# Performance work log

Measured on AMD Instinct MI355X. Metric: run time of the kernel, lower is better.

## Reference

```python
import jax, jax.numpy as jnp
import numpy as np
from jax import lax

B, T, V, D, H = 32, 128, 32000, 512, 512


def setup_inputs() -> dict:
    key = jax.random.key(0)
    ks = jax.random.split(key, 8)
    s = 0.05  # keep gate pre-activations in a sane range
    return {
        "dst": jax.random.randint(ks[0], (B, T), 0, V),
        "E": jax.random.normal(ks[1], (V, D), jnp.float32) * s,
        "W_ih": jax.random.normal(ks[2], (4 * H, D + H), jnp.float32) * s,
        "W_hh": jax.random.normal(ks[3], (4 * H, H), jnp.float32) * s,
        "b_ih": jnp.zeros((4 * H,), jnp.float32),
        "b_hh": jnp.zeros((4 * H,), jnp.float32),
        "h0": jax.random.normal(ks[4], (B, H), jnp.float32) * s,
        "c0": jax.random.normal(ks[5], (B, H), jnp.float32) * s,
        "out0": jax.random.normal(ks[6], (B, H), jnp.float32) * s,
    }


def reference(dst, E, W_ih, W_hh, b_ih, b_hh, h0, c0, out0):
    # Embed targets: [B, T, D] -> time-major [T, B, D]
    emb_tbd = jnp.swapaxes(E[dst], 0, 1)

    def step(carry, e_t):
        h, c, out_prev = carry
        # input feeding: concat embedding with previous output -> [B, D+H]
        x = jnp.concatenate([e_t, out_prev], axis=1)
        gates = x @ W_ih.T + b_ih + h @ W_hh.T + b_hh  # [B, 4H]
        i, f, g, o = jnp.split(gates, 4, axis=1)
        i = jax.nn.sigmoid(i)
        f = jax.nn.sigmoid(f)
        g = jnp.tanh(g)
        o = jax.nn.sigmoid(o)
        c_new = f * c + i * g
        h_new = o * jnp.tanh(c_new)
        # attn is identity; dropout disabled (p=0 / eval)
        return (h_new, c_new, h_new), h_new

    _, outs_tbh = lax.scan(step, (h0, c0, out0), emb_tbd)  # [T, B, H]
    out_bth = jnp.swapaxes(outs_tbh, 0, 1)  # [B, T, H]
    # weight-tied projection to vocab + log softmax
    logits = jnp.einsum("bth,vh->btv", out_bth, E)  # [B, T, V]
    return jax.nn.log_softmax(logits, axis=-1)
```

## Files before the change

### kernel.cpp

```cpp
#include <hip/hip_runtime.h>
#include <hip/hip_bf16.h>
#include <math.h>

#define B_ 32
#define T_ 128
#define V_ 32000
#define D_ 512
#define H_ 512

typedef __attribute__((ext_vector_type(8))) short bf16x8;
typedef __attribute__((ext_vector_type(4))) float f32x4;
typedef __attribute__((ext_vector_type(2))) unsigned long long u64x2;

#define AS1 __attribute__((address_space(1)))
#define AS3 __attribute__((address_space(3)))

__device__ __forceinline__ unsigned short f2bf(float x) {
  unsigned int b = __float_as_uint(x);
  return (unsigned short)((b + 0x7FFFu + ((b >> 16) & 1u)) >> 16);
}
__device__ __forceinline__ float bf2f(unsigned short u) {
  return __uint_as_float(((unsigned int)u) << 16);
}
__device__ __forceinline__ float sigm(float x) { return 1.0f / (1.0f + __expf(-x)); }
__device__ __forceinline__ float tanh_fast(float x) { return 1.0f - 2.0f / (__expf(2.0f * x) + 1.0f); }

__device__ __forceinline__ unsigned long long ald64(const unsigned long long* p) {
  return __hip_atomic_load(p, __ATOMIC_RELAXED, __HIP_MEMORY_SCOPE_AGENT);
}
__device__ __forceinline__ unsigned ald32(const unsigned* p) {
  return __hip_atomic_load(p, __ATOMIC_RELAXED, __HIP_MEMORY_SCOPE_AGENT);
}

__global__ __launch_bounds__(64) void embed_bf_kernel(const int* __restrict__ dst,
                                                      const float* __restrict__ E,
                                                      unsigned short* __restrict__ embbf) {
  int rt = blockIdx.x;
  int t = rt >> 5, b = rt & 31;
  int v = dst[b * T_ + t];
  const float4* src = (const float4*)(E + (size_t)v * D_);
  ushort4* d = (ushort4*)(embbf + (size_t)rt * D_);
  #pragma unroll
  for (int r = 0; r < 2; ++r) {
    float4 x = src[threadIdx.x + r * 64];
    ushort4 o; o.x = f2bf(x.x); o.y = f2bf(x.y); o.z = f2bf(x.z); o.w = f2bf(x.w);
    d[threadIdx.x + r * 64] = o;
  }
}

__global__ void cvt_kernel(const float* __restrict__ in, unsigned short* __restrict__ out, int n4) {
  int stride = gridDim.x * blockDim.x;
  for (int i = blockIdx.x * blockDim.x + threadIdx.x; i < n4; i += stride) {
    float4 v = ((const float4*)in)[i];
    ushort4 o; o.x = f2bf(v.x); o.y = f2bf(v.y); o.z = f2bf(v.z); o.w = f2bf(v.w);
    ((ushort4*)out)[i] = o;
  }
}

__global__ void cvt_w1_kernel(const float* __restrict__ Wih, unsigned short* __restrict__ W1bf, int n4) {
  int stride = gridDim.x * blockDim.x;
  for (int i = blockIdx.x * blockDim.x + threadIdx.x; i < n4; i += stride) {
    int flat = i * 4;
    int r = flat >> 9, c = flat & 511;
    float4 v = *(const float4*)(Wih + (size_t)r * 1024 + c);
    ushort4 o; o.x = f2bf(v.x); o.y = f2bf(v.y); o.z = f2bf(v.z); o.w = f2bf(v.w);
    ((ushort4*)W1bf)[i] = o;
  }
}

__global__ void wr_prep_swz_kernel(const float* __restrict__ Wih, const float* __restrict__ Whh,
                                   unsigned short* __restrict__ Wrs, int n4) {
  int stride = gridDim.x * blockDim.x;
  for (int i = blockIdx.x * blockDim.x + threadIdx.x; i < n4; i += stride) {
    int flat = i * 4;
    int grow = flat >> 9, k = flat & 511;
    float4 a = *(const float4*)(Wih + (size_t)grow * 1024 + 512 + k);
    float4 b = ((const float4*)Whh)[i];
    ushort4 o;
    o.x = f2bf(a.x + b.x); o.y = f2bf(a.y + b.y); o.z = f2bf(a.z + b.z); o.w = f2bf(a.w + b.w);
    int gate = grow >> 9, kgl = grow & 511;
    int orow = (kgl >> 5) * 128 + (kgl & 31) * 4 + gate;
    int chunk = (k >> 3) ^ (orow & 7);
    *(ushort4*)(Wrs + (size_t)orow * 512 + chunk * 8 + (k & 7)) = o;
  }
}

__global__ __launch_bounds__(256) void gemm_pre_kernel(
    const unsigned short* __restrict__ A,
    const unsigned short* __restrict__ Bm,
    const float* __restrict__ bih, const float* __restrict__ bhh,
    unsigned short* __restrict__ preA3)
{
  __shared__ unsigned short ldsA[2][128 * 32];
  __shared__ unsigned short ldsB[2][128 * 32];
  const int tid = threadIdx.x;
  const int lane = tid & 63;
  const int wid = tid >> 6;
  const int wm = wid >> 1, wn = wid & 1;
  const int m0 = blockIdx.y * 128;
  const int n0 = blockIdx.x * 128;
  const int srow = lane >> 2;
  const int scol = (lane & 3) * 8;

  f32x4 acc[4][4] = {};
  const int NK = 512 / 32;

  auto stage = [&](int kk, int buf) {
    const int k0 = kk * 32;
    #pragma unroll
    for (int c = 0; c < 2; ++c) {
      const int r = wid * 32 + c * 16;
      const unsigned short* sa = A  + (size_t)(m0 + r + srow) * 512 + k0 + scol;
      const unsigned short* sb = Bm + (size_t)(n0 + r + srow) * 512 + k0 + scol;
      __builtin_amdgcn_global_load_lds((const AS1 void*)sa, (AS3 void*)&ldsA[buf][r * 32], 16, 0, 0);
      __builtin_amdgcn_global_load_lds((const AS1 void*)sb, (AS3 void*)&ldsB[buf][r * 32], 16, 0, 0);
    }
  };

  stage(0, 0);
  __syncthreads();

  const int rl = lane & 15;
  const int kb = lane >> 4;

  for (int kk = 0; kk < NK; ++kk) {
    const int buf = kk & 1;
    if (kk + 1 < NK) stage(kk + 1, buf ^ 1);
    const bf16x8* Af = (const bf16x8*)&ldsA[buf][0];
    const bf16x8* Bf = (const bf16x8*)&ldsB[buf][0];
    bf16x8 av[4], bv[4];
    #pragma unroll
    for (int mi = 0; mi < 4; ++mi) av[mi] = Af[(wm * 64 + mi * 16 + rl) * 4 + kb];
    #pragma unroll
    for (int ni = 0; ni < 4; ++ni) bv[ni] = Bf[(wn * 64 + ni * 16 + rl) * 4 + kb];
    #pragma unroll
    for (int mi = 0; mi < 4; ++mi)
      #pragma unroll
      for (int ni = 0; ni < 4; ++ni)
        acc[mi][ni] = __builtin_amdgcn_mfma_f32_16x16x32_bf16(av[mi], bv[ni], acc[mi][ni], 0, 0, 0);
    __syncthreads();
  }

  const int rb = (lane >> 4) * 4;
  #pragma unroll
  for (int mi = 0; mi < 4; ++mi)
    #pragma unroll
    for (int ni = 0; ni < 4; ++ni) {
      int mbase = m0 + wm * 64 + mi * 16 + rb;
      int col   = n0 + wn * 64 + ni * 16 + rl;
      int gate = col >> 9, kg = col & 511;
      int tt = mbase >> 5, bb0 = mbase & 31;
      float bb = bih[col] + bhh[col];
      #pragma unroll
      for (int j = 0; j < 4; ++j)
        preA3[(((size_t)tt * 512 + kg) * 32 + bb0 + j) * 4 + gate] = f2bf(acc[mi][ni][j] + bb);
    }
}

__global__ __launch_bounds__(256) void delta0_kernel(const float* __restrict__ Wih,
                                                     const float* __restrict__ out0,
                                                     const float* __restrict__ h0,
                                                     unsigned short* __restrict__ preA3) {
  const int r = blockIdx.x;
  const int tid = threadIdx.x;
  const int b = tid >> 3, seg = tid & 7;
  __shared__ float red[32][9];
  const float4* o4 = (const float4*)(out0 + (size_t)b * 512 + seg * 64);
  const float4* h4 = (const float4*)(h0 + (size_t)b * 512 + seg * 64);
  const float4* w4 = (const float4*)(Wih + (size_t)r * 1024 + 512 + seg * 64);
  float s = 0.f;
  #pragma unroll
  for (int j = 0; j < 16; ++j) {
    float4 o = o4[j], h = h4[j], w = w4[j];
    s += (o.x - h.x) * w.x + (o.y - h.y) * w.y + (o.z - h.z) * w.z + (o.w - h.w) * w.w;
  }
  red[b][seg] = s;
  __syncthreads();
  if (tid < 32) {
    float t = 0.f;
    #pragma unroll
    for (int j = 0; j < 8; ++j) t += red[tid][j];
    int gate = r >> 9, kgl = r & 511;
    unsigned short* p = preA3 + ((size_t)kgl * 32 + tid) * 4 + gate;
    *p = f2bf(bf2f(*p) + t);
  }
}

__global__ __launch_bounds__(1024) void lstm_persist_rs_kernel(
    const unsigned short* __restrict__ Wrs,
    const unsigned short* __restrict__ preA3,
    const float* __restrict__ c0,
    unsigned short* __restrict__ hb0,
    unsigned short* __restrict__ hb1,
    unsigned short* __restrict__ Abf,
    unsigned int* __restrict__ flags)
{
  __shared__ unsigned short wlds[128 * 512];
  __shared__ __align__(16) char hexch[2][16 * 1024];
  const int tid = threadIdx.x, bid = blockIdx.x;
  const int lane = tid & 63, wid = tid >> 6;

  #pragma unroll
  for (int it = 0; it < 8; ++it) {
    int r = it * 16 + wid;
    const unsigned short* src = Wrs + ((size_t)bid * 128 + r) * 512 + lane * 8;
    __builtin_amdgcn_global_load_lds((const AS1 void*)src, (AS3 void*)&wlds[r * 512], 16, 0, 0);
  }

  const int myhalf = wid >> 3;
  const int rt = wid & 7;
  const int q = lane >> 4, rl = lane & 15;
  const int kg = bid * 32 + rt * 4 + q;
  const int b = myhalf * 16 + rl;
  float c_reg = c0[(size_t)b * 512 + kg];

  const int row = rt * 16 + rl;
  const char* wbase = (const char*)wlds + row * 1024;
  const int rx = (row & 7) << 4;
  const int hx = (rl & 7) << 4;

  const int sw = wid & 7;
  const int sr = sw * 2 + (lane >> 5);
  const int sc = lane & 31;
  const int sblk = sc >> 1;
  const int srx = (sr & 7) << 4;
  const int sofs = sc * 32;

  if (myhalf == 0) {
    const unsigned long long* src =
        (const unsigned long long*)(hb0 + (size_t)sr * 512) + sc * 4;
    unsigned long long d0 = ald64(src + 0), d1 = ald64(src + 1);
    unsigned long long d2 = ald64(src + 2), d3 = ald64(src + 3);
    char* dst = hexch[0] + sr * 1024;
    u64x2 w0; w0[0] = d0; w0[1] = d1;
    u64x2 w1; w1[0] = d2; w1[1] = d3;
    *(u64x2*)(dst + (sofs ^ srx)) = w0;
    *(u64x2*)(dst + ((sofs + 16) ^ srx)) = w1;
  }
  __syncthreads();

  for (int p = 0; p < 2 * T_; ++p) {
    const int t = p >> 1, ph = p & 1, buf = p & 1;

    if (myhalf == ph) {
      unsigned long long pre =
          *(const unsigned long long*)(preA3 + (((size_t)t * 512 + kg) * 32 + b) * 4);
      const char* hbase = hexch[buf] + rl * 1024;
      f32x4 acc = {}, acc2 = {};
      #pragma unroll
      for (int kk = 0; kk < 16; kk += 2) {
        int k0 = kk * 32 + q * 8;
        int k1 = k0 + 32;
        bf16x8 av0 = *(const bf16x8*)(wbase + ((k0 * 2) ^ rx));
        bf16x8 bv0 = *(const bf16x8*)(hbase + ((k0 * 2) ^ hx));
        bf16x8 av1 = *(const bf16x8*)(wbase + ((k1 * 2) ^ rx));
        bf16x8 bv1 = *(const bf16x8*)(hbase + ((k1 * 2) ^ hx));
        acc  = __builtin_amdgcn_mfma_f32_16x16x32_bf16(av0, bv0, acc, 0, 0, 0);
        acc2 = __builtin_amdgcn_mfma_f32_16x16x32_bf16(av1, bv1, acc2, 0, 0, 0);
      }
      float g0 = acc[0] + acc2[0] + bf2f((unsigned short)(pre));
      float g1 = acc[1] + acc2[1] + bf2f((unsigned short)(pre >> 16));
      float g2 = acc[2] + acc2[2] + bf2f((unsigned short)(pre >> 32));
      float g3 = acc[3] + acc2[3] + bf2f((unsigned short)(pre >> 48));
      float iv = sigm(g0), fv = sigm(g1), gv = tanh_fast(g2), ov = sigm(g3);
      float cn = fv * c_reg + iv * gv;
      c_reg = cn;
      float hn = ov * tanh_fast(cn);
      int hv = (int)f2bf(hn);
      int nb = __shfl(hv, lane + 16);
      if ((q & 1) == 0) {
        unsigned pair = (unsigned)hv | ((unsigned)nb << 16);
        if (t != T_ - 1) {
          unsigned short* hout = ((t + 1) & 1) ? hb1 : hb0;
          __hip_atomic_store((unsigned int*)(hout + (size_t)b * 512 + kg), pair,
                             __ATOMIC_RELAXED, __HIP_MEMORY_SCOPE_AGENT);
        }
        *(unsigned*)(Abf + ((size_t)b * T_ + t) * 512 + kg) = pair;
      }
    } else if (p + 1 < 2 * T_) {
      const int t2 = (p + 1) >> 1;
      if (t2 > 0) {
        const unsigned* fl = &flags[(myhalf * 16 + sblk) * 16];
        unsigned spins = 0;
        while (ald32(fl) < (unsigned)t2) {
          if (++spins > 1000000u) break;
        }
      }
      const unsigned short* hsrc = (t2 & 1) ? hb1 : hb0;
      const unsigned long long* src =
          (const unsigned long long*)(hsrc + (size_t)(myhalf * 16 + sr) * 512) + sc * 4;
      unsigned long long d0 = ald64(src + 0), d1 = ald64(src + 1);
      unsigned long long d2 = ald64(src + 2), d3 = ald64(src + 3);
      char* dst = hexch[buf ^ 1] + sr * 1024;
      u64x2 w0; w0[0] = d0; w0[1] = d1;
      u64x2 w1; w1[0] = d2; w1[1] = d3;
      *(u64x2*)(dst + (sofs ^ srx)) = w0;
      *(u64x2*)(dst + ((sofs + 16) ^ srx)) = w1;
    }

    __syncthreads();

    if (tid == ph * 512)
      __hip_atomic_store(&flags[(ph * 16 + bid) * 16], (unsigned)(t + 1),
                         __ATOMIC_RELAXED, __HIP_MEMORY_SCOPE_AGENT);
  }
}

__global__ __launch_bounds__(256) void gemm_kernel(
    const unsigned short* __restrict__ A,
    const unsigned short* __restrict__ Bm,
    float* __restrict__ C,
    float* __restrict__ pmax, float* __restrict__ psum)
{
  __shared__ unsigned short ldsA[2][128 * 32];
  __shared__ unsigned short ldsB[2][128 * 32];
  __shared__ float smax[2][128];
  __shared__ float ssum[2][128];
  const int tid = threadIdx.x;
  const int lane = tid & 63;
  const int wid = tid >> 6;
  const int wm = wid >> 1, wn = wid & 1;
  const int m0 = blockIdx.x * 128;
  const int n0 = blockIdx.y * 128;
  const int srow = lane >> 2;

  f32x4 acc[4][4] = {};
  const int NK = 512 / 32;

  auto stage = [&](int kk, int buf) {
    const int k0 = kk * 32;
    const int sw = (srow >> 1) & 3;
    const int gc = ((lane & 3) ^ sw) * 8;
    #pragma unroll
    for (int c = 0; c < 2; ++c) {
      const int r = wid * 32 + c * 16;
      const unsigned short* sa = A  + (size_t)(m0 + r + srow) * 512 + k0 + gc;
      const unsigned short* sb = Bm + (size_t)(n0 + r + srow) * 512 + k0 + gc;
      __builtin_amdgcn_global_load_lds((const AS1 void*)sa, (AS3 void*)&ldsA[buf][r * 32], 16, 0, 0);
      __builtin_amdgcn_global_load_lds((const AS1 void*)sb, (AS3 void*)&ldsB[buf][r * 32], 16, 0, 0);
    }
  };

  stage(0, 0);
  __syncthreads();

  const int rl = lane & 15;
  const int kb = lane >> 4;
  const int rsw = kb ^ ((rl >> 1) & 3);

  for (int kk = 0; kk < NK; ++kk) {
    const int buf = kk & 1;
    if (kk + 1 < NK) stage(kk + 1, buf ^ 1);
    const bf16x8* Af = (const bf16x8*)&ldsA[buf][0];
    const bf16x8* Bf = (const bf16x8*)&ldsB[buf][0];
    bf16x8 av[4], bv[4];
    #pragma unroll
    for (int mi = 0; mi < 4; ++mi) av[mi] = Af[(wm * 64 + mi * 16 + rl) * 4 + rsw];
    #pragma unroll
    for (int ni = 0; ni < 4; ++ni) bv[ni] = Bf[(wn * 64 + ni * 16 + rl) * 4 + rsw];
    #pragma unroll
    for (int mi = 0; mi < 4; ++mi)
      #pragma unroll
      for (int ni = 0; ni < 4; ++ni)
        acc[mi][ni] = __builtin_amdgcn_mfma_f32_16x16x32_bf16(av[mi], bv[ni], acc[mi][ni], 0, 0, 0);
    __syncthreads();
  }

  const int rb = kb * 4;
  #pragma unroll
  for (int mi = 0; mi < 4; ++mi)
    #pragma unroll
    for (int ni = 0; ni < 4; ++ni) {
      size_t rrow = (size_t)(m0 + wm * 64 + mi * 16 + rb);
      size_t col = (size_t)(n0 + wn * 64 + ni * 16 + rl);
      #pragma unroll
      for (int j = 0; j < 4; ++j)
        __builtin_nontemporal_store(acc[mi][ni][j], &C[(rrow + j) * (size_t)V_ + col]);
    }

  float tm[4][4];
  #pragma unroll
  for (int mi = 0; mi < 4; ++mi)
    #pragma unroll
    for (int j = 0; j < 4; ++j) {
      float m = fmaxf(fmaxf(acc[mi][0][j], acc[mi][1][j]), fmaxf(acc[mi][2][j], acc[mi][3][j]));
      m = fmaxf(m, __shfl_xor(m, 1)); m = fmaxf(m, __shfl_xor(m, 2));
      m = fmaxf(m, __shfl_xor(m, 4)); m = fmaxf(m, __shfl_xor(m, 8));
      tm[mi][j] = m;
    }
  if (rl == 0) {
    #pragma unroll
    for (int mi = 0; mi < 4; ++mi)
      #pragma unroll
      for (int j = 0; j < 4; ++j)
        smax[wn][wm * 64 + mi * 16 + kb * 4 + j] = tm[mi][j];
  }
  __syncthreads();
  float ts[4][4];
  #pragma unroll
  for (int mi = 0; mi < 4; ++mi)
    #pragma unroll
    for (int j = 0; j < 4; ++j) {
      int rlocal = wm * 64 + mi * 16 + kb * 4 + j;
      float M = fmaxf(smax[0][rlocal], smax[1][rlocal]);
      float s = __expf(acc[mi][0][j] - M) + __expf(acc[mi][1][j] - M) +
                __expf(acc[mi][2][j] - M) + __expf(acc[mi][3][j] - M);
      s += __shfl_xor(s, 1); s += __shfl_xor(s, 2);
      s += __shfl_xor(s, 4); s += __shfl_xor(s, 8);
      ts[mi][j] = s;
    }
  if (rl == 0) {
    #pragma unroll
    for (int mi = 0; mi < 4; ++mi)
      #pragma unroll
      for (int j = 0; j < 4; ++j)
        ssum[wn][wm * 64 + mi * 16 + kb * 4 + j] = ts[mi][j];
  }
  __syncthreads();
  if (tid < 128) {
    float M = fmaxf(smax[0][tid], smax[1][tid]);
    float S = ssum[0][tid] + ssum[1][tid];
    pmax[(size_t)(m0 + tid) * 256 + blockIdx.y] = M;
    psum[(size_t)(m0 + tid) * 256 + blockIdx.y] = S;
  }
}

__global__ __launch_bounds__(256) void softmax_finish_kernel(
    float* __restrict__ C, const float* __restrict__ pmax, const float* __restrict__ psum) {
  const size_t row = blockIdx.x;
  const int tid = threadIdx.x, lane = tid & 63, wid = tid >> 6;
  __shared__ float red[4];

  float pm = (tid < 250) ? pmax[row * 256 + tid] : -INFINITY;
  float ps = (tid < 250) ? psum[row * 256 + tid] : 0.f;

  float m = pm;
  #pragma unroll
  for (int off = 32; off > 0; off >>= 1) m = fmaxf(m, __shfl_xor(m, off));
  if (lane == 0) red[wid] = m;
  __syncthreads();
  m = fmaxf(fmaxf(red[0], red[1]), fmaxf(red[2], red[3]));
  __syncthreads();

  float s = (tid < 250) ? ps * __expf(pm - m) : 0.f;
  #pragma unroll
  for (int off = 32; off > 0; off >>= 1) s += __shfl_xor(s, off);
  if (lane == 0) red[wid] = s;
  __syncthreads();
  s = red[0] + red[1] + red[2] + red[3];
  const float lse = m + logf(s);

  f32x4* p4 = (f32x4*)(C + row * (size_t)V_);
  for (int i = tid; i < 8000; i += 256) {
    f32x4 v = p4[i];
    v -= lse;
    __builtin_nontemporal_store(v, &p4[i]);
  }
}

extern "C" void kernel_launch(void* const* d_in, const int* in_sizes, int n_in,
                              void* d_out, int out_size, void* d_ws, size_t ws_size,
                              hipStream_t stream) {
  const int*   dst  = (const int*)d_in[0];
  const float* E    = (const float*)d_in[1];
  const float* Wih  = (const float*)d_in[2];
  const float* Whh  = (const float*)d_in[3];
  const float* bih  = (const float*)d_in[4];
  const float* bhh  = (const float*)d_in[5];
  const float* h0   = (const float*)d_in[6];
  const float* c0   = (const float*)d_in[7];
  const float* out0 = (const float*)d_in[8];
  float* C = (float*)d_out;

  char* ws = (char*)d_ws;
  unsigned short* Ebf   = (unsigned short*)(ws);
  unsigned short* preA3 = (unsigned short*)(ws + (size_t)33554432);
  unsigned short* Wrs   = (unsigned short*)(ws + (size_t)50331648);
  unsigned short* embbf = (unsigned short*)(ws + (size_t)52428800);
  float*          pmax  = (float*)(ws + (size_t)52428800);
  unsigned short* W1bf  = (unsigned short*)(ws + (size_t)56623104);
  float*          psum  = (float*)(ws + (size_t)56623104);
  unsigned short* Abf   = (unsigned short*)(ws + (size_t)60817408);
  unsigned short* hb0   = (unsigned short*)(ws + (size_t)65011712);
  unsigned short* hb1   = (unsigned short*)(ws + (size_t)65044480);
  unsigned int*   flg   = (unsigned int*)(ws + (size_t)65077248);

  (void)hipMemsetAsync(flg, 0, 2048, stream);

  embed_bf_kernel<<<dim3(T_ * B_), dim3(64), 0, stream>>>(dst, E, embbf);
  cvt_kernel<<<dim3(2048), dim3(256), 0, stream>>>(E, Ebf, V_ * D_ / 4);
  cvt_w1_kernel<<<dim3(256), dim3(256), 0, stream>>>(Wih, W1bf, 2048 * 512 / 4);
  wr_prep_swz_kernel<<<dim3(256), dim3(256), 0, stream>>>(Wih, Whh, Wrs, 2048 * 512 / 4);

  gemm_pre_kernel<<<dim3(2048 / 128, 4096 / 128), dim3(256), 0, stream>>>(embbf, W1bf, bih, bhh, preA3);
  delta0_kernel<<<dim3(2048), dim3(256), 0, stream>>>(Wih, out0, h0, preA3);
  cvt_kernel<<<dim3(16), dim3(256), 0, stream>>>(h0, hb0, B_ * H_ / 4);

  lstm_persist_rs_kernel<<<dim3(16), dim3(1024), 0, stream>>>(Wrs, preA3, c0, hb0, hb1, Abf, flg);

  gemm_kernel<<<dim3(32, 250), dim3(256), 0, stream>>>(Abf, Ebf, C, pmax, psum);
  softmax_finish_kernel<<<dim3(B_ * T_), dim3(256), 0, stream>>>(C, pmax, psum);
}
```

Before: 1.082 ms.

## Fuse LSTM recurrence and vocab projection into one flag-synchronized mega kernel

Merges the persistent LSTM kernel and the vocab GEMM into one launch. The first 16 blocks run the recurrence, and the remaining blocks spin on the per-step flags until the 8 timesteps covering their 256-row time-major tile of the hidden output are done, then compute logits and partial softmax stats. This lets the output projection overlap the serial recurrence instead of waiting for it to finish. The tradeoffs are a time-major hidden layout with remapped output rows, 1024-thread GEMM blocks with a different tile shape and plain global-to-LDS staging, and a dependence on the recurrence blocks being scheduled before the spinning blocks, which risks deadlock or starvation.

```diff
diff --git a/kernel.cpp b/kernel.cpp
--- a/kernel.cpp
+++ b/kernel.cpp
@@ -186,253 +186,251 @@
   }
 }
 
-__global__ __launch_bounds__(1024) void lstm_persist_rs_kernel(
+__global__ __launch_bounds__(1024) void mega_kernel(
     const unsigned short* __restrict__ Wrs,
     const unsigned short* __restrict__ preA3,
     const float* __restrict__ c0,
     unsigned short* __restrict__ hb0,
     unsigned short* __restrict__ hb1,
     unsigned short* __restrict__ Abf,
-    unsigned int* __restrict__ flags)
+    unsigned int* __restrict__ flags,
+    const unsigned short* __restrict__ Ebf,
+    float* __restrict__ C,
+    float* __restrict__ pmax, float* __restrict__ psum)
 {
-  __shared__ unsigned short wlds[128 * 512];
-  __shared__ __align__(16) char hexch[2][16 * 1024];
+  __shared__ __align__(16) char smem[163840];
   const int tid = threadIdx.x, bid = blockIdx.x;
   const int lane = tid & 63, wid = tid >> 6;
 
-  #pragma unroll
-  for (int it = 0; it < 8; ++it) {
-    int r = it * 16 + wid;
-    const unsigned short* src = Wrs + ((size_t)bid * 128 + r) * 512 + lane * 8;
-    __builtin_amdgcn_global_load_lds((const AS1 void*)src, (AS3 void*)&wlds[r * 512], 16, 0, 0);
-  }
-
-  const int myhalf = wid >> 3;
-  const int rt = wid & 7;
-  const int q = lane >> 4, rl = lane & 15;
-  const int kg = bid * 32 + rt * 4 + q;
-  const int b = myhalf * 16 + rl;
-  float c_reg = c0[(size_t)b * 512 + kg];
-
-  const int row = rt * 16 + rl;
-  const char* wbase = (const char*)wlds + row * 1024;
-  const int rx = (row & 7) << 4;
-  const int hx = (rl & 7) << 4;
-
-  const int sw = wid & 7;
-  const int sr = sw * 2 + (lane >> 5);
-  const int sc = lane & 31;
-  const int sblk = sc >> 1;
-  const int srx = (sr & 7) << 4;
-  const int sofs = sc * 32;
-
-  if (myhalf == 0) {
-    const unsigned long long* src =
-        (const unsigned long long*)(hb0 + (size_t)sr * 512) + sc * 4;
-    unsigned long long d0 = ald64(src + 0), d1 = ald64(src + 1);
-    unsigned long long d2 = ald64(src + 2), d3 = ald64(src + 3);
-    char* dst = hexch[0] + sr * 1024;
-    u64x2 w0; w0[0] = d0; w0[1] = d1;
-    u64x2 w1; w1[0] = d2; w1[1] = d3;
-    *(u64x2*)(dst + (sofs ^ srx)) = w0;
-    *(u64x2*)(dst + ((sofs + 16) ^ srx)) = w1;
-  }
-  __syncthreads();
-
-  for (int p = 0; p < 2 * T_; ++p) {
-    const int t = p >> 1, ph = p & 1, buf = p & 1;
-
-    if (myhalf == ph) {
-      unsigned long long pre =
-          *(const unsigned long long*)(preA3 + (((size_t)t * 512 + kg) * 32 + b) * 4);
-      const char* hbase = hexch[buf] + rl * 1024;
-      f32x4 acc = {}, acc2 = {};
-      #pragma unroll
-      for (int kk = 0; kk < 16; kk += 2) {
-        int k0 = kk * 32 + q * 8;
-        int k1 = k0 + 32;
-        bf16x8 av0 = *(const bf16x8*)(wbase + ((k0 * 2) ^ rx));
-        bf16x8 bv0 = *(const bf16x8*)(hbase + ((k0 * 2) ^ hx));
-        bf16x8 av1 = *(const bf16x8*)(wbase + ((k1 * 2) ^ rx));
-        bf16x8 bv1 = *(const bf16x8*)(hbase + ((k1 * 2) ^ hx));
-        acc  = __builtin_amdgcn_mfma_f32_16x16x32_bf16(av0, bv0, acc, 0, 0, 0);
-        acc2 = __builtin_amdgcn_mfma_f32_16x16x32_bf16(av1, bv1, acc2, 0, 0, 0);
-      }
-      float g0 = acc[0] + acc2[0] + bf2f((unsigned short)(pre));
-      float g1 = acc[1] + acc2[1] + bf2f((unsigned short)(pre >> 16));
-      float g2 = acc[2] + acc2[2] + bf2f((unsigned short)(pre >> 32));
-      float g3 = acc[3] + acc2[3] + bf2f((unsigned short)(pre >> 48));
-      float iv = sigm(g0), fv = sigm(g1), gv = tanh_fast(g2), ov = sigm(g3);
-      float cn = fv * c_reg + iv * gv;
-      c_reg = cn;
-      float hn = ov * tanh_fast(cn);
-      int hv = (int)f2bf(hn);
-      int nb = __shfl(hv, lane + 16);
-      if ((q & 1) == 0) {
-        unsigned pair = (unsigned)hv | ((unsigned)nb << 16);
-        if (t != T_ - 1) {
-          unsigned short* hout = ((t + 1) & 1) ? hb1 : hb0;
-          __hip_atomic_store((unsigned int*)(hout + (size_t)b * 512 + kg), pair,
-                             __ATOMIC_RELAXED, __HIP_MEMORY_SCOPE_AGENT);
-        }
-        *(unsigned*)(Abf + ((size_t)b * T_ + t) * 512 + kg) = pair;
-      }
-    } else if (p + 1 < 2 * T_) {
-      const int t2 = (p + 1) >> 1;
-      if (t2 > 0) {
-        const unsigned* fl = &flags[(myhalf * 16 + sblk) * 16];
-        unsigned spins = 0;
-        while (ald32(fl) < (unsigned)t2) {
-          if (++spins > 1000000u) break;
-        }
-      }
-      const unsigned short* hsrc = (t2 & 1) ? hb1 : hb0;
+  if (bid < 16) {
+    unsigned short* wlds = (unsigned short*)smem;
+    char* hx = smem + 131072;
+
+    #pragma unroll
+    for (int it = 0; it < 8; ++it) {
+      int r = it * 16 + wid;
+      const unsigned short* src = Wrs + ((size_t)bid * 128 + r) * 512 + lane * 8;
+      __builtin_amdgcn_global_load_lds((const AS1 void*)src, (AS3 void*)&wlds[r * 512], 16, 0, 0);
+    }
+
+    const int myhalf = wid >> 3;
+    const int rt = wid & 7;
+    const int q = lane >> 4, rl = lane & 15;
+    const int kg = bid * 32 + rt * 4 + q;
+    const int b = myhalf * 16 + rl;
+    float c_reg = c0[(size_t)b * 512 + kg];
+
+    const int row = rt * 16 + rl;
+    const char* wbase = (const char*)wlds + row * 1024;
+    const int rx = (row & 7) << 4;
+    const int hxs = (rl & 7) << 4;
+
+    const int sw = wid & 7;
+    const int sr = sw * 2 + (lane >> 5);
+    const int sc = lane & 31;
+    const int sblk = sc >> 1;
+    const int srx = (sr & 7) << 4;
+    const int sofs = sc * 32;
+
+    if (myhalf == 0) {
       const unsigned long long* src =
-          (const unsigned long long*)(hsrc + (size_t)(myhalf * 16 + sr) * 512) + sc * 4;
+          (const unsigned long long*)(hb0 + (size_t)sr * 512) + sc * 4;
       unsigned long long d0 = ald64(src + 0), d1 = ald64(src + 1);
       unsigned long long d2 = ald64(src + 2), d3 = ald64(src + 3);
-      char* dst = hexch[buf ^ 1] + sr * 1024;
+      char* dst = hx + sr * 1024;
       u64x2 w0; w0[0] = d0; w0[1] = d1;
       u64x2 w1; w1[0] = d2; w1[1] = d3;
       *(u64x2*)(dst + (sofs ^ srx)) = w0;
       *(u64x2*)(dst + ((sofs + 16) ^ srx)) = w1;
     }
-
     __syncthreads();
 
-    if (tid == ph * 512)
-      __hip_atomic_store(&flags[(ph * 16 + bid) * 16], (unsigned)(t + 1),
-                         __ATOMIC_RELAXED, __HIP_MEMORY_SCOPE_AGENT);
-  }
-}
-
-__global__ __launch_bounds__(256) void gemm_kernel(
-    const unsigned short* __restrict__ A,
-    const unsigned short* __restrict__ Bm,
-    float* __restrict__ C,
-    float* __restrict__ pmax, float* __restrict__ psum)
-{
-  __shared__ unsigned short ldsA[2][128 * 32];
-  __shared__ unsigned short ldsB[2][128 * 32];
-  __shared__ float smax[2][128];
-  __shared__ float ssum[2][128];
-  const int tid = threadIdx.x;
-  const int lane = tid & 63;
-  const int wid = tid >> 6;
-  const int wm = wid >> 1, wn = wid & 1;
-  const int m0 = blockIdx.x * 128;
-  const int n0 = blockIdx.y * 128;
-  const int srow = lane >> 2;
-
-  f32x4 acc[4][4] = {};
-  const int NK = 512 / 32;
-
-  auto stage = [&](int kk, int buf) {
-    const int k0 = kk * 32;
-    const int sw = (srow >> 1) & 3;
-    const int gc = ((lane & 3) ^ sw) * 8;
-    #pragma unroll
-    for (int c = 0; c < 2; ++c) {
-      const int r = wid * 32 + c * 16;
-      const unsigned short* sa = A  + (size_t)(m0 + r + srow) * 512 + k0 + gc;
-      const unsigned short* sb = Bm + (size_t)(n0 + r + srow) * 512 + k0 + gc;
-      __builtin_amdgcn_global_load_lds((const AS1 void*)sa, (AS3 void*)&ldsA[buf][r * 32], 16, 0, 0);
-      __builtin_amdgcn_global_load_lds((const AS1 void*)sb, (AS3 void*)&ldsB[buf][r * 32], 16, 0, 0);
+    for (int p = 0; p < 2 * T_; ++p) {
+      const int t = p >> 1, ph = p & 1, buf = p & 1;
+
+      if (myhalf == ph) {
+        unsigned long long pre =
+            *(const unsigned long long*)(preA3 + (((size_t)t * 512 + kg) * 32 + b) * 4);
+        const char* hbase = hx + buf * 16384 + rl * 1024;
+        f32x4 acc = {}, acc2 = {};
+        #pragma unroll
+        for (int kk = 0; kk < 16; kk += 2) {
+          int k0 = kk * 32 + q * 8;
+          int k1 = k0 + 32;
+          bf16x8 av0 = *(const bf16x8*)(wbase + ((k0 * 2) ^ rx));
+          bf16x8 bv0 = *(const bf16x8*)(hbase + ((k0 * 2) ^ hxs));
+          bf16x8 av1 = *(const bf16x8*)(wbase + ((k1 * 2) ^ rx));
+          bf16x8 bv1 = *(const bf16x8*)(hbase + ((k1 * 2) ^ hxs));
+          acc  = __builtin_amdgcn_mfma_f32_16x16x32_bf16(av0, bv0, acc, 0, 0, 0);
+          acc2 = __builtin_amdgcn_mfma_f32_16x16x32_bf16(av1, bv1, acc2, 0, 0, 0);
+        }
+        float g0 = acc[0] + acc2[0] + bf2f((unsigned short)(pre));
+        float g1 = acc[1] + acc2[1] + bf2f((unsigned short)(pre >> 16));
+        float g2 = acc[2] + acc2[2] + bf2f((unsigned short)(pre >> 32));
+        float g3 = acc[3] + acc2[3] + bf2f((unsigned short)(pre >> 48));
+        float iv = sigm(g0), fv = sigm(g1), gv = tanh_fast(g2), ov = sigm(g3);
+        float cn = fv * c_reg + iv * gv;
+        c_reg = cn;
+        float hn = ov * tanh_fast(cn);
+        int hv = (int)f2bf(hn);
+        int nb = __shfl(hv, lane + 16);
+        if ((q & 1) == 0) {
+          unsigned pair = (unsigned)hv | ((unsigned)nb << 16);
+          if (t != T_ - 1) {
+            unsigned short* hout = ((t + 1) & 1) ? hb1 : hb0;
+            __hip_atomic_store((unsigned int*)(hout + (size_t)b * 512 + kg), pair,
+                               __ATOMIC_RELAXED, __HIP_MEMORY_SCOPE_AGENT);
+          }
+          __hip_atomic_store((unsigned int*)(Abf + ((size_t)t * 32 + b) * 512 + kg), pair,
+                             __ATOMIC_RELAXED, __HIP_MEMORY_SCOPE_AGENT);
+        }
+      } else if (p + 1 < 2 * T_) {
+        const int t2 = (p + 1) >> 1;
+        if (t2 > 0) {
+          const unsigned* fl = &flags[(myhalf * 16 + sblk) * 16];
+          unsigned spins = 0;
+          while (ald32(fl) < (unsigned)t2) {
+            if (++spins > 1000000u) break;
+          }
+        }
+        const unsigned short* hsrc = (t2 & 1) ? hb1 : hb0;
+        const unsigned long long* src =
+            (const unsigned long long*)(hsrc + (size_t)(myhalf * 16 + sr) * 512) + sc * 4;
+        unsigned long long d0 = ald64(src + 0), d1 = ald64(src + 1);
+        unsigned long long d2 = ald64(src + 2), d3 = ald64(src + 3);
+        char* dst = hx + (buf ^ 1) * 16384 + sr * 1024;
+        u64x2 w0; w0[0] = d0; w0[1] = d1;
+        u64x2 w1; w1[0] = d2; w1[1] = d3;
+        *(u64x2*)(dst + (sofs ^ srx)) = w0;
+        *(u64x2*)(dst + ((sofs + 16) ^ srx)) = w1;
+      }
+
+      __syncthreads();
+
+      if (tid == ph * 512)
+        __hip_atomic_store(&flags[(ph * 16 + bid) * 16], (unsigned)(t + 1),
+                           __ATOMIC_RELAXED, __HIP_MEMORY_SCOPE_AGENT);
+    }
+    return;
+  }
+
+  const int e = bid - 16;
+  const int n_t = e % 250, m_t = e / 250;
+  const int m0 = m_t * 256, n0 = n_t * 128;
+
+  if (tid < 32) {
+    const unsigned want = (unsigned)(8 * m_t + 8);
+    unsigned spins = 0;
+    while (ald32(&flags[tid * 16]) < want) {
+      __builtin_amdgcn_s_sleep(2);
+      if (++spins > 2000000u) break;
+    }
+  }
+  __syncthreads();
+
+  unsigned short* Al[2] = { (unsigned short*)smem, (unsigned short*)(smem + 20480) };
+  unsigned short* Bb[2] = { (unsigned short*)(smem + 40960), (unsigned short*)(smem + 51200) };
+  float (*smax)[256] = (float (*)[256])(smem + 61440);
+  float (*ssum)[256] = (float (*)[256])(smem + 65536);
+
+  const int trow = tid >> 2, tcol = tid & 3;
+  const int wm = wid >> 2, wn = wid & 3;
+  const int rl = lane & 15, kb = lane >> 4;
+
+  auto stageP = [&](int kk, int bf) {
+    {
+      const unsigned long long* src =
+          (const unsigned long long*)(Abf + (size_t)(m0 + trow) * 512 + kk * 32 + tcol * 8);
+      unsigned long long d0 = ald64(src), d1 = ald64(src + 1);
+      u64x2 w; w[0] = d0; w[1] = d1;
+      *(u64x2*)((char*)Al[bf] + trow * 80 + tcol * 16) = w;
+    }
+    if (tid < 512) {
+      int br = tid >> 2, bc = tid & 3;
+      u64x2 w = *(const u64x2*)(Ebf + (size_t)(n0 + br) * 512 + kk * 32 + bc * 8);
+      *(u64x2*)((char*)Bb[bf] + br * 80 + bc * 16) = w;
     }
   };
 
-  stage(0, 0);
-  __syncthreads();
-
-  const int rl = lane & 15;
-  const int kb = lane >> 4;
-  const int rsw = kb ^ ((rl >> 1) & 3);
-
-  for (int kk = 0; kk < NK; ++kk) {
-    const int buf = kk & 1;
-    if (kk + 1 < NK) stage(kk + 1, buf ^ 1);
-    const bf16x8* Af = (const bf16x8*)&ldsA[buf][0];
-    const bf16x8* Bf = (const bf16x8*)&ldsB[buf][0];
-    bf16x8 av[4], bv[4];
-    #pragma unroll
-    for (int mi = 0; mi < 4; ++mi) av[mi] = Af[(wm * 64 + mi * 16 + rl) * 4 + rsw];
-    #pragma unroll
-    for (int ni = 0; ni < 4; ++ni) bv[ni] = Bf[(wn * 64 + ni * 16 + rl) * 4 + rsw];
-    #pragma unroll
-    for (int mi = 0; mi < 4; ++mi)
+  f32x4 acc[4][2] = {};
+  stageP(0, 0);
+  __syncthreads();
+
+  for (int kk = 0; kk < 16; ++kk) {
+    const int bf = kk & 1;
+    if (kk + 1 < 16) stageP(kk + 1, bf ^ 1);
+    bf16x8 bv[2];
+    #pragma unroll
+    for (int y = 0; y < 2; ++y) {
+      int br = wn * 32 + y * 16 + rl;
+      bv[y] = *(const bf16x8*)((char*)Bb[bf] + br * 80 + kb * 16);
+    }
+    #pragma unroll
+    for (int x = 0; x < 4; ++x) {
+      int ar = wm * 64 + x * 16 + rl;
+      bf16x8 av = *(const bf16x8*)((char*)Al[bf] + ar * 80 + kb * 16);
       #pragma unroll
-      for (int ni = 0; ni < 4; ++ni)
-        acc[mi][ni] = __builtin_amdgcn_mfma_f32_16x16x32_bf16(av[mi], bv[ni], acc[mi][ni], 0, 0, 0);
+      for (int y = 0; y < 2; ++y)
+        acc[x][y] = __builtin_amdgcn_mfma_f32_16x16x32_bf16(av, bv[y], acc[x][y], 0, 0, 0);
+    }
     __syncthreads();
   }
 
-  const int rb = kb * 4;
-  #pragma unroll
-  for (int mi = 0; mi < 4; ++mi)
-    #pragma unroll
-    for (int ni = 0; ni < 4; ++ni) {
-      size_t rrow = (size_t)(m0 + wm * 64 + mi * 16 + rb);
-      size_t col = (size_t)(n0 + wn * 64 + ni * 16 + rl);
+  #pragma unroll
+  for (int x = 0; x < 4; ++x)
+    #pragma unroll
+    for (int y = 0; y < 2; ++y) {
+      int col = n0 + wn * 32 + y * 16 + rl;
       #pragma unroll
-      for (int j = 0; j < 4; ++j)
-        __builtin_nontemporal_store(acc[mi][ni][j], &C[(rrow + j) * (size_t)V_ + col]);
-    }
-
-  float tm[4][4];
-  #pragma unroll
-  for (int mi = 0; mi < 4; ++mi)
+      for (int j = 0; j < 4; ++j) {
+        int arow = m0 + wm * 64 + x * 16 + kb * 4 + j;
+        size_t crow = (size_t)(arow & 31) * T_ + (arow >> 5);
+        __builtin_nontemporal_store(acc[x][y][j], &C[crow * (size_t)V_ + col]);
+      }
+    }
+
+  #pragma unroll
+  for (int x = 0; x < 4; ++x)
     #pragma unroll
     for (int j = 0; j < 4; ++j) {
-      float m = fmaxf(fmaxf(acc[mi][0][j], acc[mi][1][j]), fmaxf(acc[mi][2][j], acc[mi][3][j]));
+      float m = fmaxf(acc[x][0][j], acc[x][1][j]);
       m = fmaxf(m, __shfl_xor(m, 1)); m = fmaxf(m, __shfl_xor(m, 2));
       m = fmaxf(m, __shfl_xor(m, 4)); m = fmaxf(m, __shfl_xor(m, 8));
-      tm[mi][j] = m;
-    }
-  if (rl == 0) {
-    #pragma unroll
-    for (int mi = 0; mi < 4; ++mi)
-      #pragma unroll
-      for (int j = 0; j < 4; ++j)
-        smax[wn][wm * 64 + mi * 16 + kb * 4 + j] = tm[mi][j];
-  }
-  __syncthreads();
-  float ts[4][4];
-  #pragma unroll
-  for (int mi = 0; mi < 4; ++mi)
+      if (rl == 0) smax[wn][wm * 64 + x * 16 + kb * 4 + j] = m;
+    }
+  __syncthreads();
+  #pragma unroll
+  for (int x = 0; x < 4; ++x)
     #pragma unroll
     for (int j = 0; j < 4; ++j) {
-      int rlocal = wm * 64 + mi * 16 + kb * 4 + j;
-      float M = fmaxf(smax[0][rlocal], smax[1][rlocal]);
-      float s = __expf(acc[mi][0][j] - M) + __expf(acc[mi][1][j] - M) +
-                __expf(acc[mi][2][j] - M) + __expf(acc[mi][3][j] - M);
+      int rowl = wm * 64 + x * 16 + kb * 4 + j;
+      float M = fmaxf(fmaxf(smax[0][rowl], smax[1][rowl]),
+                      fmaxf(smax[2][rowl], smax[3][rowl]));
+      float s = __expf(acc[x][0][j] - M) + __expf(acc[x][1][j] - M);
       s += __shfl_xor(s, 1); s += __shfl_xor(s, 2);
       s += __shfl_xor(s, 4); s += __shfl_xor(s, 8);
-      ts[mi][j] = s;
-    }
-  if (rl == 0) {
-    #pragma unroll
-    for (int mi = 0; mi < 4; ++mi)
-      #pragma unroll
-      for (int j = 0; j < 4; ++j)
-        ssum[wn][wm * 64 + mi * 16 + kb * 4 + j] = ts[mi][j];
-  }
-  __syncthreads();
-  if (tid < 128) {
-    float M = fmaxf(smax[0][tid], smax[1][tid]);
-    float S = ssum[0][tid] + ssum[1][tid];
-    pmax[(size_t)(m0 + tid) * 256 + blockIdx.y] = M;
-    psum[(size_t)(m0 + tid) * 256 + blockIdx.y] = S;
+      if (rl == 0) ssum[wn][rowl] = s;
+    }
+  __syncthreads();
+  if (tid < 256) {
+    float M = fmaxf(fmaxf(smax[0][tid], smax[1][tid]),
+                    fmaxf(smax[2][tid], smax[3][tid]));
+    float S = ssum[0][tid] + ssum[1][tid] + ssum[2][tid] + ssum[3][tid];
+    pmax[(size_t)(m0 + tid) * 256 + n_t] = M;
+    psum[(size_t)(m0 + tid) * 256 + n_t] = S;
   }
 }
 
 __global__ __launch_bounds__(256) void softmax_finish_kernel(
     float* __restrict__ C, const float* __restrict__ pmax, const float* __restrict__ psum) {
   const size_t row = blockIdx.x;
+  const int b = blockIdx.x >> 7, t = blockIdx.x & 127;
+  const size_t arow = (size_t)t * 32 + b;
   const int tid = threadIdx.x, lane = tid & 63, wid = tid >> 6;
   __shared__ float red[4];
 
-  float pm = (tid < 250) ? pmax[row * 256 + tid] : -INFINITY;
-  float ps = (tid < 250) ? psum[row * 256 + tid] : 0.f;
+  float pm = (tid < 250) ? pmax[arow * 256 + tid] : -INFINITY;
+  float ps = (tid < 250) ? psum[arow * 256 + tid] : 0.f;
 
   float m = pm;
   #pragma unroll
@@ -496,8 +494,8 @@
   delta0_kernel<<<dim3(2048), dim3(256), 0, stream>>>(Wih, out0, h0, preA3);
   cvt_kernel<<<dim3(16), dim3(256), 0, stream>>>(h0, hb0, B_ * H_ / 4);
 
-  lstm_persist_rs_kernel<<<dim3(16), dim3(1024), 0, stream>>>(Wrs, preA3, c0, hb0, hb1, Abf, flg);
-
-  gemm_kernel<<<dim3(32, 250), dim3(256), 0, stream>>>(Abf, Ebf, C, pmax, psum);
+  mega_kernel<<<dim3(16 + 16 * 250), dim3(1024), 0, stream>>>(
+      Wrs, preA3, c0, hb0, hb1, Abf, flg, Ebf, C, pmax, psum);
+
   softmax_finish_kernel<<<dim3(B_ * T_), dim3(256), 0, stream>>>(C, pmax, psum);
 }
```

Result: faster. 989.2 us (-8.6%).
